# Optimization experiments

Measured on AMD Instinct MI355X. Metric: run time of the kernel, lower is better.

The kernel has to match this reference:

```python
import jax, jax.numpy as jnp
import numpy as np

B, T, N, CD, D = 8, 16, 256, 1280, 1024   # batch, frames, feats/frame, condition_dim, dim
H, DH, DEPTH, Q = 16, 64, 6, 16           # heads, dim_head, depth, latents per frame
FF = 4 * D


def setup_inputs() -> dict:
    key = jax.random.key(0)
    ks = iter(jax.random.split(key, 40))
    w = lambda shp: jax.random.normal(next(ks), shp, jnp.float32) * 0.02
    return dict(
        x_f=jax.random.normal(next(ks), (B, T, N, CD), jnp.float32),
        goal_w1=w((CD, 2 * D)), goal_b1=jnp.zeros((2 * D,), jnp.float32),
        goal_w2=w((2 * D, D)), goal_b2=jnp.zeros((D,), jnp.float32),
        latents=jax.random.normal(next(ks), (T, Q, D), jnp.float32),
        time_pos_emb=jax.random.normal(next(ks), (T, 1, D), jnp.float32),
        ln_media_g=jnp.ones((DEPTH, D), jnp.float32), ln_media_b=jnp.zeros((DEPTH, D), jnp.float32),
        ln_lat_g=jnp.ones((DEPTH, D), jnp.float32), ln_lat_b=jnp.zeros((DEPTH, D), jnp.float32),
        wq=w((DEPTH, D, H * DH)), wk=w((DEPTH, D, H * DH)), wv=w((DEPTH, D, H * DH)),
        wo=w((DEPTH, H * DH, D)),
        ffn_ln_g=jnp.ones((DEPTH, D), jnp.float32), ffn_ln_b=jnp.zeros((DEPTH, D), jnp.float32),
        ffn_w1=w((DEPTH, D, FF)), ffn_b1=jnp.zeros((DEPTH, FF), jnp.float32),
        ffn_w2=w((DEPTH, FF, D)), ffn_b2=jnp.zeros((DEPTH, D), jnp.float32),
        final_g=jnp.ones((D,), jnp.float32), final_b=jnp.zeros((D,), jnp.float32),
    )


def layer_norm(x, g, b, eps=1e-5):
    m = jnp.mean(x, axis=-1, keepdims=True)
    v = jnp.mean(jnp.square(x - m), axis=-1, keepdims=True)
    return (x - m) * jax.lax.rsqrt(v + eps) * g + b


def reference(x_f, goal_w1, goal_b1, goal_w2, goal_b2, latents, time_pos_emb,
              ln_media_g, ln_media_b, ln_lat_g, ln_lat_b, wq, wk, wv, wo,
              ffn_ln_g, ffn_ln_b, ffn_w1, ffn_b1, ffn_w2, ffn_b2, final_g, final_b):
    scale = DH ** -0.5
    # goal embedding: Linear -> GELU(exact) -> Linear, then add time positional embedding
    h = jax.nn.gelu(x_f @ goal_w1 + goal_b1, approximate=False) @ goal_w2 + goal_b2  # (B,T,N,D)
    h = h + time_pos_emb[None]                                                       # (T,1,D) broadcast
    feats = h.reshape(B * T, N, D)
    x = jnp.broadcast_to(latents[None], (B, T, Q, D)).reshape(B * T, Q, D)
    for i in range(DEPTH):
        f = layer_norm(feats, ln_media_g[i], ln_media_b[i])
        lat = layer_norm(x, ln_lat_g[i], ln_lat_b[i])
        q = (lat @ wq[i]).reshape(B * T, Q, H, DH).transpose(0, 2, 1, 3) * scale  # bhqd
        kv = jnp.concatenate([f, lat], axis=1)                                    # (BT, N+Q, D)
        k = (kv @ wk[i]).reshape(B * T, N + Q, H, DH).transpose(0, 2, 1, 3)       # bhfd
        v = (kv @ wv[i]).reshape(B * T, N + Q, H, DH).transpose(0, 2, 1, 3)
        sim = jnp.einsum('bhqd,bhfd->bhqf', q, k)
        alphas = jax.nn.softmax(sim, axis=-1)  # matches amax-subtract + softmax
        o = jnp.einsum('bhqf,bhfd->bhqd', alphas, v)
        o = o.transpose(0, 2, 1, 3).reshape(B * T, Q, H * DH)
        x = x + o @ wo[i]
        y = layer_norm(x, ffn_ln_g[i], ffn_ln_b[i])
        x = x + jax.nn.gelu(y @ ffn_w1[i] + ffn_b1[i], approximate=False) @ ffn_w2[i] + ffn_b2[i]
    x = x.reshape(B, T * Q, D)
    return layer_norm(x, final_g, final_b)
```

## Files before the change

kernel.cpp:

```cpp
#include <hip/hip_runtime.h>
#include <math.h>

#define DEV __device__ __forceinline__

typedef __attribute__((ext_vector_type(8))) short short8;
typedef __attribute__((ext_vector_type(4))) short short4v;
typedef __attribute__((ext_vector_type(4))) float f32x4;
typedef __attribute__((ext_vector_type(8))) __bf16 bf16x8;

DEV float bf2f(unsigned short u) {
    union { unsigned int i; float f; } c; c.i = ((unsigned int)u) << 16; return c.f;
}
DEV unsigned short f2bf(float f) {
    union { float f; unsigned int i; } c; c.f = f;
    unsigned int u = c.i;
    u += 0x7fffu + ((u >> 16) & 1u);
    return (unsigned short)(u >> 16);
}
DEV float gelu_exact(float x) { return 0.5f * x * (1.0f + erff(x * 0.70710678118654752f)); }

#define GLL16(g, l)                                                                   \
    __builtin_amdgcn_global_load_lds(                                                \
        (const __attribute__((address_space(1))) unsigned int*)(g),                  \
        (__attribute__((address_space(3))) unsigned int*)(l), 16, 0, 0)

__global__ __launch_bounds__(256)
void transpose_w(const float* __restrict__ in, unsigned short* __restrict__ out,
                 const float* __restrict__ rowscale, float uscale,
                 int K, int N, size_t inStride, size_t outStride, int scaleStride)
{
    __shared__ float tile[64][65];
    in  += (size_t)blockIdx.z * inStride;
    out += (size_t)blockIdx.z * outStride;
    const int k0 = blockIdx.y * 64, n0 = blockIdx.x * 64;
    const int tid = threadIdx.x;
    const int c = tid & 63;
#pragma unroll
    for (int i = 0; i < 16; ++i) {
        int rr = (i << 2) + (tid >> 6);
        float v = in[(size_t)(k0 + rr) * N + n0 + c];
        if (rowscale) v *= rowscale[(size_t)blockIdx.z * scaleStride + k0 + rr];
        tile[rr][c] = v * uscale;
    }
    __syncthreads();
#pragma unroll
    for (int i = 0; i < 16; ++i) {
        int rr = (i << 2) + (tid >> 6);
        out[(size_t)(n0 + rr) * K + k0 + c] = f2bf(tile[c][rr]);
    }
}

__global__ __launch_bounds__(256)
void fold_bias(const float* __restrict__ wk, const float* __restrict__ wv,
               const float* __restrict__ bmed, float* __restrict__ biaskv)
{
    const int d = blockIdx.x >> 3;
    const int rem = blockIdx.x & 7;
    const int part = rem >> 2;
    const int chunk = rem & 3;
    const float* w = (part ? wv : wk) + (size_t)d * 1024 * 1024 + chunk * 256 + threadIdx.x;
    const float* b = bmed + d * 1024;
    float acc = 0.f;
    for (int r = 0; r < 1024; ++r) acc += b[r] * w[(size_t)r * 1024];
    biaskv[d * 2048 + part * 1024 + chunk * 256 + threadIdx.x] = acc;
}

__global__ __launch_bounds__(256)
void convert_bf16(const float* __restrict__ in, unsigned short* __restrict__ out, size_t n4)
{
    size_t i = (size_t)blockIdx.x * 256 + threadIdx.x;
    if (i >= n4) return;
    float4 v = ((const float4*)in)[i];
    ushort4 u;
    u.x = f2bf(v.x); u.y = f2bf(v.y); u.z = f2bf(v.z); u.w = f2bf(v.w);
    ((ushort4*)out)[i] = u;
}

__global__ __launch_bounds__(256)
void init_x(const float* __restrict__ lat, float* __restrict__ x)
{
    const int row = blockIdx.x;
    ((float4*)x)[(size_t)row * 256 + threadIdx.x] =
        ((const float4*)lat)[(size_t)(row & 255) * 256 + threadIdx.x];
}

template<bool AFFINE, bool OUTBF>
__global__ __launch_bounds__(256)
void ln_k(const float* __restrict__ in, const float* __restrict__ g,
          const float* __restrict__ b, void* __restrict__ out)
{
    const int row = blockIdx.x;
    const int tid = threadIdx.x;
    float4 v = ((const float4*)(in + (size_t)row * 1024))[tid];
    float s  = v.x + v.y + v.z + v.w;
    float ss = v.x * v.x + v.y * v.y + v.z * v.z + v.w * v.w;
#pragma unroll
    for (int o = 32; o > 0; o >>= 1) { s += __shfl_down(s, o); ss += __shfl_down(ss, o); }
    __shared__ float red[8];
    if ((tid & 63) == 0) { red[tid >> 6] = s; red[4 + (tid >> 6)] = ss; }
    __syncthreads();
    const float sum  = red[0] + red[1] + red[2] + red[3];
    const float ssum = red[4] + red[5] + red[6] + red[7];
    const float mean = sum * (1.0f / 1024.0f);
    const float var  = ssum * (1.0f / 1024.0f) - mean * mean;
    const float rs   = rsqrtf(var + 1e-5f);
    float o0 = (v.x - mean) * rs, o1 = (v.y - mean) * rs;
    float o2 = (v.z - mean) * rs, o3 = (v.w - mean) * rs;
    if (AFFINE) {
        float4 gv = ((const float4*)g)[tid];
        float4 bv = ((const float4*)b)[tid];
        o0 = o0 * gv.x + bv.x; o1 = o1 * gv.y + bv.y;
        o2 = o2 * gv.z + bv.z; o3 = o3 * gv.w + bv.w;
    }
    if (OUTBF) {
        ushort4 u; u.x = f2bf(o0); u.y = f2bf(o1); u.z = f2bf(o2); u.w = f2bf(o3);
        ((ushort4*)out)[(size_t)row * 256 + tid] = u;
    } else {
        float4 ov; ov.x = o0; ov.y = o1; ov.z = o2; ov.w = o3;
        ((float4*)out)[(size_t)row * 256 + tid] = ov;
    }
}

enum { E_BF16 = 0, E_BIAS_BF16, E_BIAS_GELU_BF16, E_BIAS_TPOS_F32, E_ADD_F32, E_BIAS_ADD_F32 };

template<int EPI>
__global__ __launch_bounds__(256, 2)
void gemm_bt(const unsigned short* __restrict__ A, const unsigned short* __restrict__ Bt,
             void* __restrict__ Out,
             const float* __restrict__ bias, const float* __restrict__ addsrc,
             const float* __restrict__ tpos,
             int M, int N, int K)
{
    __shared__ unsigned short lds[2 * 128 * 64];
    const int tid  = threadIdx.x;
    const int wave = tid >> 6, lane = tid & 63;
    const int nbx  = N >> 7;

    const int nwg = gridDim.x;
    int bid = blockIdx.x;
    int wg = ((nwg & 7) == 0) ? ((bid & 7) * (nwg >> 3) + (bid >> 3)) : bid;
    const int by = wg / nbx, bx = wg % nbx;

    const int swz = ((lane & 7) ^ (lane >> 3)) * 8;
    const unsigned short* gA = A  + (size_t)(by * 128 + (lane >> 3)) * K + swz;
    const unsigned short* gB = Bt + (size_t)(bx * 128 + (lane >> 3)) * K + swz;

    const int wr = wave >> 1, wc = wave & 1;
    f32x4 acc[4][4] = {};

    unsigned short* ldsA = lds;
    unsigned short* ldsB = lds + 128 * 64;

    const int off0 = (((lane >> 4)    ) ^ (lane & 7)) * 8;
    const int off1 = (((lane >> 4) | 4) ^ (lane & 7)) * 8;
    const unsigned short* la = ldsA + (wr * 64 + (lane & 15)) * 64;
    const unsigned short* lb = ldsB + (wc * 64 + (lane & 15)) * 64;

    for (int kt = 0; kt < K; kt += 64) {
#pragma unroll
        for (int j = 0; j < 4; ++j) {
            const int chunk = (j << 2) + wave;
            GLL16(gA + (size_t)chunk * 8 * K + kt, ldsA + chunk * 512);
            GLL16(gB + (size_t)chunk * 8 * K + kt, ldsB + chunk * 512);
        }
        __syncthreads();
#pragma unroll
        for (int kk = 0; kk < 2; ++kk) {
            const int offk = kk ? off1 : off0;
            bf16x8 a[4], b[4];
#pragma unroll
            for (int m = 0; m < 4; ++m) a[m] = *(const bf16x8*)(la + m * 1024 + offk);
#pragma unroll
            for (int n = 0; n < 4; ++n) b[n] = *(const bf16x8*)(lb + n * 1024 + offk);
#pragma unroll
            for (int m = 0; m < 4; ++m)
#pragma unroll
                for (int n = 0; n < 4; ++n)
                    acc[m][n] = __builtin_amdgcn_mfma_f32_16x16x32_bf16(a[m], b[n], acc[m][n], 0, 0, 0);
        }
        __syncthreads();
    }

    const int r0 = by * 128 + wr * 64 + (lane >> 4) * 4;
    const int c0 = bx * 128 + wc * 64 + (lane & 15);
#pragma unroll
    for (int m = 0; m < 4; ++m) {
#pragma unroll
        for (int n = 0; n < 4; ++n) {
            const int c = c0 + n * 16;
#pragma unroll
            for (int j = 0; j < 4; ++j) {
                const int r = r0 + m * 16 + j;
                float v = acc[m][n][j];
                if (EPI == E_BIAS_BF16 || EPI == E_BIAS_GELU_BF16 ||
                    EPI == E_BIAS_TPOS_F32 || EPI == E_BIAS_ADD_F32)
                    v += bias[c];
                if (EPI == E_BIAS_GELU_BF16) v = gelu_exact(v);
                if (EPI == E_BIAS_TPOS_F32)  v += tpos[(((unsigned)r >> 8) & 15) * 1024 + c];
                if (EPI == E_ADD_F32 || EPI == E_BIAS_ADD_F32) v += addsrc[(size_t)r * N + c];
                if (EPI == E_BIAS_TPOS_F32 || EPI == E_ADD_F32 || EPI == E_BIAS_ADD_F32)
                    ((float*)Out)[(size_t)r * N + c] = v;
                else
                    ((unsigned short*)Out)[(size_t)r * N + c] = f2bf(v);
            }
        }
    }
}

template<int EPI>
__global__ __launch_bounds__(256, 4)
void gemm64(const unsigned short* __restrict__ A, const unsigned short* __restrict__ Bt,
            void* __restrict__ Out,
            const float* __restrict__ bias, const float* __restrict__ addsrc,
            int M, int N, int K)
{
    __shared__ unsigned short lds[64 * 64 + 128 * 64];
    const int tid  = threadIdx.x;
    const int wave = tid >> 6, lane = tid & 63;
    const int nbx  = N >> 7;

    const int nwg = gridDim.x;
    int bid = blockIdx.x;
    int wg = ((nwg & 7) == 0) ? ((bid & 7) * (nwg >> 3) + (bid >> 3)) : bid;
    const int by = wg / nbx, bx = wg % nbx;

    const int swz = ((lane & 7) ^ (lane >> 3)) * 8;
    const unsigned short* gA = A  + (size_t)(by * 64  + (lane >> 3)) * K + swz;
    const unsigned short* gB = Bt + (size_t)(bx * 128 + (lane >> 3)) * K + swz;

    const int wr = wave >> 1, wc = wave & 1;
    f32x4 acc[2][4] = {};

    unsigned short* ldsA = lds;
    unsigned short* ldsB = lds + 64 * 64;

    const int off0 = (((lane >> 4)    ) ^ (lane & 7)) * 8;
    const int off1 = (((lane >> 4) | 4) ^ (lane & 7)) * 8;
    const unsigned short* la = ldsA + (wr * 32 + (lane & 15)) * 64;
    const unsigned short* lb = ldsB + (wc * 64 + (lane & 15)) * 64;

    for (int kt = 0; kt < K; kt += 64) {
        GLL16(gA + (size_t)(wave)     * 8 * K + kt, ldsA + (wave)      * 512);
        GLL16(gA + (size_t)(4 + wave) * 8 * K + kt, ldsA + (4 + wave)  * 512);
#pragma unroll
        for (int j = 0; j < 4; ++j) {
            const int chunk = (j << 2) + wave;
            GLL16(gB + (size_t)chunk * 8 * K + kt, ldsB + chunk * 512);
        }
        __syncthreads();
#pragma unroll
        for (int kk = 0; kk < 2; ++kk) {
            const int offk = kk ? off1 : off0;
            bf16x8 a[2], b[4];
#pragma unroll
            for (int m = 0; m < 2; ++m) a[m] = *(const bf16x8*)(la + m * 1024 + offk);
#pragma unroll
            for (int n = 0; n < 4; ++n) b[n] = *(const bf16x8*)(lb + n * 1024 + offk);
#pragma unroll
            for (int m = 0; m < 2; ++m)
#pragma unroll
                for (int n = 0; n < 4; ++n)
                    acc[m][n] = __builtin_amdgcn_mfma_f32_16x16x32_bf16(a[m], b[n], acc[m][n], 0, 0, 0);
        }
        __syncthreads();
    }

    const int r0 = by * 64 + wr * 32 + (lane >> 4) * 4;
    const int c0 = bx * 128 + wc * 64 + (lane & 15);
#pragma unroll
    for (int m = 0; m < 2; ++m) {
#pragma unroll
        for (int n = 0; n < 4; ++n) {
            const int c = c0 + n * 16;
#pragma unroll
            for (int j = 0; j < 4; ++j) {
                const int r = r0 + m * 16 + j;
                float v = acc[m][n][j];
                if (EPI == E_BIAS_BF16 || EPI == E_BIAS_GELU_BF16 || EPI == E_BIAS_ADD_F32)
                    v += bias[c];
                if (EPI == E_BIAS_GELU_BF16) v = gelu_exact(v);
                if (EPI == E_ADD_F32 || EPI == E_BIAS_ADD_F32) v += addsrc[(size_t)r * N + c];
                if (EPI == E_ADD_F32 || EPI == E_BIAS_ADD_F32)
                    ((float*)Out)[(size_t)r * N + c] = v;
                else
                    ((unsigned short*)Out)[(size_t)r * N + c] = f2bf(v);
            }
        }
    }
}

__global__ __launch_bounds__(256)
void attn_k(const unsigned short* __restrict__ qkvl, const unsigned short* __restrict__ kvm,
            unsigned short* __restrict__ o)
{
    __shared__ unsigned short kv[272 * 72];
    __shared__ float sim[16 * 273];
    __shared__ float qs[16 * 68];
    __shared__ float red[64];

    const int bt = blockIdx.x >> 4, h = blockIdx.x & 15;
    const int tid = threadIdx.x;
    const int lane = tid & 63, wave = tid >> 6;
    const int r = tid & 15, grp = tid >> 4;

    {
        const int qi = tid >> 4, d0 = (tid & 15) * 4;
        const unsigned short* src = qkvl + (size_t)(bt * 16 + qi) * 3072 + h * 64 + d0;
        qs[qi * 68 + d0 + 0] = bf2f(src[0]);
        qs[qi * 68 + d0 + 1] = bf2f(src[1]);
        qs[qi * 68 + d0 + 2] = bf2f(src[2]);
        qs[qi * 68 + d0 + 3] = bf2f(src[3]);
    }
#pragma unroll
    for (int i = 0; i < 9; ++i) {
        int idx = i * 256 + tid;
        if (idx < 2176) {
            int f = idx >> 3, cp = idx & 7;
            const unsigned short* src = (f < 256)
                ? kvm  + (size_t)(bt * 256 + f) * 2048 + h * 64 + cp * 8
                : qkvl + (size_t)(bt * 16 + (f - 256)) * 3072 + 1024 + h * 64 + cp * 8;
            *(short8*)&kv[f * 72 + cp * 8] = *(const short8*)src;
        }
    }
    __syncthreads();

    float p[17];
#pragma unroll
    for (int i = 0; i < 17; ++i) p[i] = 0.f;
#pragma unroll
    for (int d = 0; d < 64; d += 8) {
        float q8[8];
#pragma unroll
        for (int j = 0; j < 8; ++j) q8[j] = qs[r * 68 + d + j];
#pragma unroll
        for (int i = 0; i < 17; ++i) {
            short8 k8 = *(const short8*)&kv[(grp + i * 16) * 72 + d];
#pragma unroll
            for (int j = 0; j < 8; ++j) p[i] += q8[j] * bf2f((unsigned short)k8[j]);
        }
    }
    float mx = -3.0e38f;
#pragma unroll
    for (int i = 0; i < 17; ++i) mx = fmaxf(mx, p[i]);
    mx = fmaxf(mx, __shfl_xor(mx, 16));
    mx = fmaxf(mx, __shfl_xor(mx, 32));
    if (lane < 16) red[wave * 16 + lane] = mx;
    __syncthreads();
    const float rowmax = fmaxf(fmaxf(red[r], red[16 + r]), fmaxf(red[32 + r], red[48 + r]));

    float sm = 0.f;
#pragma unroll
    for (int i = 0; i < 17; ++i) { p[i] = __expf(p[i] - rowmax); sm += p[i]; }
    sm += __shfl_xor(sm, 16);
    sm += __shfl_xor(sm, 32);
#pragma unroll
    for (int i = 0; i < 17; ++i) sim[r * 273 + grp + i * 16] = p[i];
    __syncthreads();
    if (lane < 16) red[wave * 16 + lane] = sm;
#pragma unroll
    for (int i = 0; i < 9; ++i) {
        int idx = i * 256 + tid;
        if (idx < 2176) {
            int f = idx >> 3, cp = idx & 7;
            const unsigned short* src = (f < 256)
                ? kvm  + (size_t)(bt * 256 + f) * 2048 + 1024 + h * 64 + cp * 8
                : qkvl + (size_t)(bt * 16 + (f - 256)) * 3072 + 2048 + h * 64 + cp * 8;
            *(short8*)&kv[f * 72 + cp * 8] = *(const short8*)src;
        }
    }
    __syncthreads();
    const float inv = 1.0f / (red[r] + red[16 + r] + red[32 + r] + red[48 + r]);

    float o0 = 0.f, o1 = 0.f, o2 = 0.f, o3 = 0.f;
    for (int f = 0; f < 272; ++f) {
        float pv = sim[r * 273 + f];
        short4v v4 = *(const short4v*)&kv[f * 72 + grp * 4];
        o0 += pv * bf2f((unsigned short)v4[0]);
        o1 += pv * bf2f((unsigned short)v4[1]);
        o2 += pv * bf2f((unsigned short)v4[2]);
        o3 += pv * bf2f((unsigned short)v4[3]);
    }
    unsigned short* dst = o + (size_t)(bt * 16 + r) * 1024 + h * 64 + grp * 4;
    dst[0] = f2bf(o0 * inv);
    dst[1] = f2bf(o1 * inv);
    dst[2] = f2bf(o2 * inv);
    dst[3] = f2bf(o3 * inv);
}

extern "C" void kernel_launch(void* const* d_in, const int* in_sizes, int n_in,
                              void* d_out, int out_size, void* d_ws, size_t ws_size,
                              hipStream_t stream)
{
    const float* x_f      = (const float*)d_in[0];
    const float* goal_w1  = (const float*)d_in[1];
    const float* goal_b1  = (const float*)d_in[2];
    const float* goal_w2  = (const float*)d_in[3];
    const float* goal_b2  = (const float*)d_in[4];
    const float* latents  = (const float*)d_in[5];
    const float* tpos     = (const float*)d_in[6];
    const float* lnm_g    = (const float*)d_in[7];
    const float* lnm_b    = (const float*)d_in[8];
    const float* lnl_g    = (const float*)d_in[9];
    const float* lnl_b    = (const float*)d_in[10];
    const float* wq       = (const float*)d_in[11];
    const float* wk       = (const float*)d_in[12];
    const float* wv       = (const float*)d_in[13];
    const float* wo       = (const float*)d_in[14];
    const float* ffn_g    = (const float*)d_in[15];
    const float* ffn_b    = (const float*)d_in[16];
    const float* ffw1     = (const float*)d_in[17];
    const float* ffb1     = (const float*)d_in[18];
    const float* ffw2     = (const float*)d_in[19];
    const float* ffb2     = (const float*)d_in[20];
    const float* fin_g    = (const float*)d_in[21];
    const float* fin_b    = (const float*)d_in[22];

    char* ws = (char*)d_ws;
    size_t off = 0;
    auto alloc = [&](size_t bytes) -> char* {
        char* p = ws + off;
        off += (bytes + 255) & ~(size_t)255;
        return p;
    };
    typedef unsigned short u16;
    u16*   wg1t   = (u16*)  alloc(2048ull * 1280 * 2);
    u16*   wg2t   = (u16*)  alloc(1024ull * 2048 * 2);
    u16*   wqkvl  = (u16*)  alloc(6ull * 3072 * 1024 * 2);
    u16*   wkvm   = (u16*)  alloc(6ull * 2048 * 1024 * 2);
    u16*   wot    = (u16*)  alloc(6ull * 1024 * 1024 * 2);
    u16*   wf1t   = (u16*)  alloc(6ull * 4096 * 1024 * 2);
    u16*   wf2t   = (u16*)  alloc(6ull * 1024 * 4096 * 2);
    float* biaskv = (float*)alloc(6ull * 2048 * 4);
    float* xres   = (float*)alloc(2048ull * 1024 * 4);
    u16*   latn   = (u16*)  alloc(2048ull * 1024 * 2);
    u16*   qkvl   = (u16*)  alloc(2048ull * 3072 * 2);
    u16*   obuf   = (u16*)  alloc(2048ull * 1024 * 2);
    u16*   ffny   = (u16*)  alloc(2048ull * 1024 * 2);
    u16*   ffnmid = (u16*)  alloc(2048ull * 4096 * 2);
    u16*   bufA   = (u16*)  alloc(32768ull * 2048 * 2);
    float* bufB   = (float*)alloc(32768ull * 1024 * 4);
    u16*   bufC   = (u16*)  alloc(41943040ull * 2);
    if (off > ws_size) return;

    convert_bf16<<<40960, 256, 0, stream>>>(x_f, bufC, 41943040ull / 4);
    transpose_w<<<dim3(32, 20, 1), 256, 0, stream>>>(goal_w1, wg1t, nullptr, 1.f, 1280, 2048, 0, 0, 0);
    transpose_w<<<dim3(16, 32, 1), 256, 0, stream>>>(goal_w2, wg2t, nullptr, 1.f, 2048, 1024, 0, 0, 0);
    transpose_w<<<dim3(16, 16, 6), 256, 0, stream>>>(wq, wqkvl,                nullptr, 0.125f, 1024, 1024, 1024ull*1024, 3072ull*1024, 0);
    transpose_w<<<dim3(16, 16, 6), 256, 0, stream>>>(wk, wqkvl + 1024ull*1024, nullptr, 1.f,    1024, 1024, 1024ull*1024, 3072ull*1024, 0);
    transpose_w<<<dim3(16, 16, 6), 256, 0, stream>>>(wv, wqkvl + 2048ull*1024, nullptr, 1.f,    1024, 1024, 1024ull*1024, 3072ull*1024, 0);
    transpose_w<<<dim3(16, 16, 6), 256, 0, stream>>>(wk, wkvm,                 lnm_g,   1.f,    1024, 1024, 1024ull*1024, 2048ull*1024, 1024);
    transpose_w<<<dim3(16, 16, 6), 256, 0, stream>>>(wv, wkvm + 1024ull*1024,  lnm_g,   1.f,    1024, 1024, 1024ull*1024, 2048ull*1024, 1024);
    transpose_w<<<dim3(16, 16, 6), 256, 0, stream>>>(wo, wot,                  nullptr, 1.f,    1024, 1024, 1024ull*1024, 1024ull*1024, 0);
    transpose_w<<<dim3(64, 16, 6), 256, 0, stream>>>(ffw1, wf1t,               nullptr, 1.f,    1024, 4096, 4096ull*1024, 4096ull*1024, 0);
    transpose_w<<<dim3(16, 64, 6), 256, 0, stream>>>(ffw2, wf2t,               nullptr, 1.f,    4096, 1024, 4096ull*1024, 4096ull*1024, 0);
    fold_bias<<<48, 256, 0, stream>>>(wk, wv, lnm_b, biaskv);
    init_x<<<2048, 256, 0, stream>>>(latents, xres);

    gemm_bt<E_BIAS_GELU_BF16><<<256 * 16, 256, 0, stream>>>(bufC, wg1t, bufA, goal_b1, nullptr, nullptr, 32768, 2048, 1280);
    gemm_bt<E_BIAS_TPOS_F32><<<256 * 8, 256, 0, stream>>>(bufA, wg2t, bufB, goal_b2, nullptr, tpos, 32768, 1024, 2048);
    ln_k<false, true><<<32768, 256, 0, stream>>>(bufB, nullptr, nullptr, bufC);

    for (int i = 0; i < 6; ++i) {
        const u16* wqkvl_i = wqkvl + (size_t)i * 3072 * 1024;
        const u16* wkvm_i  = wkvm  + (size_t)i * 2048 * 1024;
        const u16* wot_i   = wot   + (size_t)i * 1024 * 1024;
        const u16* wf1_i   = wf1t  + (size_t)i * 4096 * 1024;
        const u16* wf2_i   = wf2t  + (size_t)i * 1024 * 4096;

        ln_k<true, true><<<2048, 256, 0, stream>>>(xres, lnl_g + i * 1024, lnl_b + i * 1024, latn);
        gemm64<E_BF16><<<32 * 24, 256, 0, stream>>>(latn, wqkvl_i, qkvl, nullptr, nullptr, 2048, 3072, 1024);
        gemm_bt<E_BIAS_BF16><<<256 * 16, 256, 0, stream>>>(bufC, wkvm_i, bufA, biaskv + i * 2048, nullptr, nullptr, 32768, 2048, 1024);
        attn_k<<<2048, 256, 0, stream>>>(qkvl, bufA, obuf);
        gemm64<E_ADD_F32><<<32 * 8, 256, 0, stream>>>(obuf, wot_i, xres, nullptr, xres, 2048, 1024, 1024);
        ln_k<true, true><<<2048, 256, 0, stream>>>(xres, ffn_g + i * 1024, ffn_b + i * 1024, ffny);
        gemm64<E_BIAS_GELU_BF16><<<32 * 32, 256, 0, stream>>>(ffny, wf1_i, ffnmid, ffb1 + i * 4096, nullptr, 2048, 4096, 1024);
        gemm64<E_BIAS_ADD_F32><<<32 * 8, 256, 0, stream>>>(ffnmid, wf2_i, xres, ffb2 + i * 1024, xres, 2048, 1024, 4096);
    }

    ln_k<true, false><<<2048, 256, 0, stream>>>(xres, fin_g, fin_b, d_out);
}
```

Measured before the change: 2.825 ms.

## Replace 128x128 GEMM with 256x256 eight-wave ping-pong pipelined GEMM

Replaces the large-M bf16 GEMM kernel (goal embedding and per-layer media K/V projections) with a 256x256-tile, 512-thread kernel. It double-buffers LDS with async global-to-LDS loads issued two k-tiles ahead, splits each k-step into four phases with barriers and raised MFMA priority, and hoists the bias load out of the inner epilogue loop. The goal is to overlap memory traffic with MFMA work and raise arithmetic intensity. In exchange it uses 128KB of LDS and more accumulator registers per thread, which may limit occupancy. The hand-placed vmcnt waits also have to be exactly right for correctness.

```diff
diff --git a/kernel.cpp b/kernel.cpp
--- a/kernel.cpp
+++ b/kernel.cpp
@@ -19,10 +19,17 @@
 }
 DEV float gelu_exact(float x) { return 0.5f * x * (1.0f + erff(x * 0.70710678118654752f)); }
 
+DEV f32x4 MF(bf16x8 a, bf16x8 b, f32x4 c) {
+    return __builtin_amdgcn_mfma_f32_16x16x32_bf16(a, b, c, 0, 0, 0);
+}
+
 #define GLL16(g, l)                                                                   \
     __builtin_amdgcn_global_load_lds(                                                \
         (const __attribute__((address_space(1))) unsigned int*)(g),                  \
         (__attribute__((address_space(3))) unsigned int*)(l), 16, 0, 0)
+
+#define BAR()   __builtin_amdgcn_s_barrier()
+#define LGKM0() asm volatile("s_waitcnt lgkmcnt(0)" ::: "memory")
 
 __global__ __launch_bounds__(256)
 void transpose_w(const float* __restrict__ in, unsigned short* __restrict__ out,
@@ -124,84 +131,137 @@
 enum { E_BF16 = 0, E_BIAS_BF16, E_BIAS_GELU_BF16, E_BIAS_TPOS_F32, E_ADD_F32, E_BIAS_ADD_F32 };
 
 template<int EPI>
-__global__ __launch_bounds__(256, 2)
-void gemm_bt(const unsigned short* __restrict__ A, const unsigned short* __restrict__ Bt,
-             void* __restrict__ Out,
-             const float* __restrict__ bias, const float* __restrict__ addsrc,
-             const float* __restrict__ tpos,
-             int M, int N, int K)
-{
-    __shared__ unsigned short lds[2 * 128 * 64];
-    const int tid  = threadIdx.x;
-    const int wave = tid >> 6, lane = tid & 63;
-    const int nbx  = N >> 7;
-
+__global__ __launch_bounds__(512, 2)
+void g8p(const unsigned short* __restrict__ A, const unsigned short* __restrict__ Bt,
+         void* __restrict__ Out,
+         const float* __restrict__ bias, const float* __restrict__ tpos,
+         int M, int N, int K)
+{
+    __shared__ unsigned short sm[65536];
+
+    const int tid = threadIdx.x;
+    const int wid = tid >> 6, lane = tid & 63;
+    const int wm = wid >> 2, wn = wid & 3;
+
+    const int nbx = N >> 8;
     const int nwg = gridDim.x;
-    int bid = blockIdx.x;
-    int wg = ((nwg & 7) == 0) ? ((bid & 7) * (nwg >> 3) + (bid >> 3)) : bid;
+    const int bid = blockIdx.x;
+    const int wg = (bid & 7) * (nwg >> 3) + (bid >> 3);
     const int by = wg / nbx, bx = wg % nbx;
-
-    const int swz = ((lane & 7) ^ (lane >> 3)) * 8;
-    const unsigned short* gA = A  + (size_t)(by * 128 + (lane >> 3)) * K + swz;
-    const unsigned short* gB = Bt + (size_t)(bx * 128 + (lane >> 3)) * K + swz;
-
-    const int wr = wave >> 1, wc = wave & 1;
-    f32x4 acc[4][4] = {};
-
-    unsigned short* ldsA = lds;
-    unsigned short* ldsB = lds + 128 * 64;
-
-    const int off0 = (((lane >> 4)    ) ^ (lane & 7)) * 8;
-    const int off1 = (((lane >> 4) | 4) ^ (lane & 7)) * 8;
-    const unsigned short* la = ldsA + (wr * 64 + (lane & 15)) * 64;
-    const unsigned short* lb = ldsB + (wc * 64 + (lane & 15)) * 64;
-
-    for (int kt = 0; kt < K; kt += 64) {
-#pragma unroll
-        for (int j = 0; j < 4; ++j) {
-            const int chunk = (j << 2) + wave;
-            GLL16(gA + (size_t)chunk * 8 * K + kt, ldsA + chunk * 512);
-            GLL16(gB + (size_t)chunk * 8 * K + kt, ldsB + chunk * 512);
-        }
-        __syncthreads();
-#pragma unroll
-        for (int kk = 0; kk < 2; ++kk) {
-            const int offk = kk ? off1 : off0;
-            bf16x8 a[4], b[4];
-#pragma unroll
-            for (int m = 0; m < 4; ++m) a[m] = *(const bf16x8*)(la + m * 1024 + offk);
-#pragma unroll
-            for (int n = 0; n < 4; ++n) b[n] = *(const bf16x8*)(lb + n * 1024 + offk);
-#pragma unroll
-            for (int m = 0; m < 4; ++m)
-#pragma unroll
-                for (int n = 0; n < 4; ++n)
-                    acc[m][n] = __builtin_amdgcn_mfma_f32_16x16x32_bf16(a[m], b[n], acc[m][n], 0, 0, 0);
-        }
-        __syncthreads();
-    }
-
-    const int r0 = by * 128 + wr * 64 + (lane >> 4) * 4;
-    const int c0 = bx * 128 + wc * 64 + (lane & 15);
-#pragma unroll
-    for (int m = 0; m < 4; ++m) {
-#pragma unroll
-        for (int n = 0; n < 4; ++n) {
-            const int c = c0 + n * 16;
+    const int nt = K >> 6;
+
+    const int srow = wid * 8 + (lane >> 3);
+    const int schk = ((lane & 7) ^ (lane >> 3)) * 8;
+    const unsigned short* gA = A  + (size_t)(by * 256 + srow) * K + schk;
+    const unsigned short* gB = Bt + (size_t)(bx * 256 + srow) * K + schk;
+    const int ldst = wid * 512;
+
+    auto stgA = [&](int d, int h, int T) {
+        const unsigned short* g = gA + (size_t)(h * 64) * K + (size_t)T * 64;
+        unsigned short* l = sm + d * 16384 + h * 8192 + ldst;
+        GLL16(g, l);
+        GLL16(g + (size_t)128 * K, l + 4096);
+    };
+    auto stgB = [&](int d, int h, int T) {
+        const unsigned short* g = gB + (size_t)(h * 128) * K + (size_t)T * 64;
+        unsigned short* l = sm + 32768 + d * 16384 + h * 8192 + ldst;
+        GLL16(g, l);
+        GLL16(g + (size_t)64 * K, l + 4096);
+    };
+
+    const int q = lane >> 4;
+    const int cks0 = ((q    ) ^ (lane & 7)) * 8;
+    const int cks1 = ((q + 4) ^ (lane & 7)) * 8;
+    const int arow = (wm * 64 + (lane & 15)) * 64;
+    const int brow = ((wn & 1) * 64 + (lane & 15)) * 64;
+    const int bhoff = 32768 + (wn >> 1) * 8192;
+
+    f32x4 acc[8][4] = {};
+    bf16x8 a[2][2], b[4][2];
+
+    stgA(0, 0, 0); stgA(0, 1, 0); stgB(0, 0, 0); stgB(0, 1, 0);
+    if (nt > 1) { stgB(1, 0, 1); stgA(1, 0, 1); }
+    if (nt > 1) asm volatile("s_waitcnt vmcnt(4)" ::: "memory");
+    else        asm volatile("s_waitcnt vmcnt(0)" ::: "memory");
+    BAR();
+
+#define PH_READ_A(HOFF, E0)                                                      \
+    a[0][0] = *(const bf16x8*)(Ab + (HOFF) + arow + (E0) * 1024 + cks0);         \
+    a[0][1] = *(const bf16x8*)(Ab + (HOFF) + arow + (E0) * 1024 + cks1);         \
+    a[1][0] = *(const bf16x8*)(Ab + (HOFF) + arow + ((E0) + 1) * 1024 + cks0);   \
+    a[1][1] = *(const bf16x8*)(Ab + (HOFF) + arow + ((E0) + 1) * 1024 + cks1);
+
+#define PH_MFMA(R0)                                                              \
+    __builtin_amdgcn_s_setprio(1);                                               \
+    _Pragma("unroll")                                                            \
+    for (int e = 0; e < 2; ++e)                                                  \
+        _Pragma("unroll")                                                        \
+        for (int ni = 0; ni < 4; ++ni) {                                         \
+            acc[(R0) + e][ni] = MF(a[e][0], b[ni][0], acc[(R0) + e][ni]);        \
+            acc[(R0) + e][ni] = MF(a[e][1], b[ni][1], acc[(R0) + e][ni]);        \
+        }                                                                        \
+    __builtin_amdgcn_s_setprio(0);
+
+    for (int T = 0; T < nt; ++T) {
+        const int d = T & 1, dn = d ^ 1;
+        const unsigned short* Ab = sm + d * 16384;
+        const unsigned short* Bb = sm + bhoff + d * 16384;
+        const bool s1 = (T + 1 < nt), s2 = (T + 2 < nt);
+
+        PH_READ_A(0, 0);
+#pragma unroll
+        for (int ni = 0; ni < 4; ++ni) {
+            b[ni][0] = *(const bf16x8*)(Bb + brow + ni * 1024 + cks0);
+            b[ni][1] = *(const bf16x8*)(Bb + brow + ni * 1024 + cks1);
+        }
+        if (s1) { stgB(dn, 1, T + 1); stgA(dn, 1, T + 1); }
+        BAR(); LGKM0();
+        PH_MFMA(0);
+        BAR();
+
+        PH_READ_A(0, 2);
+        if (s2) stgB(d, 0, T + 2);
+        BAR(); LGKM0();
+        PH_MFMA(2);
+        BAR();
+
+        PH_READ_A(8192, 0);
+        if (s2) stgA(d, 0, T + 2);
+        BAR(); LGKM0();
+        PH_MFMA(4);
+        BAR();
+
+        PH_READ_A(8192, 2);
+        BAR(); LGKM0();
+        PH_MFMA(6);
+        if (s2)      asm volatile("s_waitcnt vmcnt(4)" ::: "memory");
+        else if (s1) asm volatile("s_waitcnt vmcnt(0)" ::: "memory");
+        BAR();
+    }
+#undef PH_READ_A
+#undef PH_MFMA
+
+    const int r0 = by * 256 + wm * 128 + (lane >> 4) * 4;
+    const int c0 = bx * 256 + wn * 64 + (lane & 15);
+#pragma unroll
+    for (int mi = 0; mi < 8; ++mi) {
+#pragma unroll
+        for (int ni = 0; ni < 4; ++ni) {
+            const int c = c0 + ni * 16;
+            float bv = 0.f;
+            if (EPI == E_BIAS_BF16 || EPI == E_BIAS_GELU_BF16 || EPI == E_BIAS_TPOS_F32)
+                bv = bias[c];
 #pragma unroll
             for (int j = 0; j < 4; ++j) {
-                const int r = r0 + m * 16 + j;
-                float v = acc[m][n][j];
-                if (EPI == E_BIAS_BF16 || EPI == E_BIAS_GELU_BF16 ||
-                    EPI == E_BIAS_TPOS_F32 || EPI == E_BIAS_ADD_F32)
-                    v += bias[c];
+                const int r = r0 + mi * 16 + j;
+                float v = acc[mi][ni][j] + bv;
                 if (EPI == E_BIAS_GELU_BF16) v = gelu_exact(v);
-                if (EPI == E_BIAS_TPOS_F32)  v += tpos[(((unsigned)r >> 8) & 15) * 1024 + c];
-                if (EPI == E_ADD_F32 || EPI == E_BIAS_ADD_F32) v += addsrc[(size_t)r * N + c];
-                if (EPI == E_BIAS_TPOS_F32 || EPI == E_ADD_F32 || EPI == E_BIAS_ADD_F32)
+                if (EPI == E_BIAS_TPOS_F32) {
+                    v += tpos[(((unsigned)r >> 8) & 15) * 1024 + c];
                     ((float*)Out)[(size_t)r * N + c] = v;
-                else
+                } else {
                     ((unsigned short*)Out)[(size_t)r * N + c] = f2bf(v);
+                }
             }
         }
     }
@@ -456,8 +516,8 @@
     fold_bias<<<48, 256, 0, stream>>>(wk, wv, lnm_b, biaskv);
     init_x<<<2048, 256, 0, stream>>>(latents, xres);
 
-    gemm_bt<E_BIAS_GELU_BF16><<<256 * 16, 256, 0, stream>>>(bufC, wg1t, bufA, goal_b1, nullptr, nullptr, 32768, 2048, 1280);
-    gemm_bt<E_BIAS_TPOS_F32><<<256 * 8, 256, 0, stream>>>(bufA, wg2t, bufB, goal_b2, nullptr, tpos, 32768, 1024, 2048);
+    g8p<E_BIAS_GELU_BF16><<<1024, 512, 0, stream>>>(bufC, wg1t, bufA, goal_b1, nullptr, 32768, 2048, 1280);
+    g8p<E_BIAS_TPOS_F32><<<512, 512, 0, stream>>>(bufA, wg2t, bufB, goal_b2, tpos, 32768, 1024, 2048);
     ln_k<false, true><<<32768, 256, 0, stream>>>(bufB, nullptr, nullptr, bufC);
 
     for (int i = 0; i < 6; ++i) {
@@ -469,7 +529,7 @@
 
         ln_k<true, true><<<2048, 256, 0, stream>>>(xres, lnl_g + i * 1024, lnl_b + i * 1024, latn);
         gemm64<E_BF16><<<32 * 24, 256, 0, stream>>>(latn, wqkvl_i, qkvl, nullptr, nullptr, 2048, 3072, 1024);
-        gemm_bt<E_BIAS_BF16><<<256 * 16, 256, 0, stream>>>(bufC, wkvm_i, bufA, biaskv + i * 2048, nullptr, nullptr, 32768, 2048, 1024);
+        g8p<E_BIAS_BF16><<<1024, 512, 0, stream>>>(bufC, wkvm_i, bufA, biaskv + i * 2048, nullptr, 32768, 2048, 1024);
         attn_k<<<2048, 256, 0, stream>>>(qkvl, bufA, obuf);
         gemm64<E_ADD_F32><<<32 * 8, 256, 0, stream>>>(obuf, wot_i, xres, nullptr, xres, 2048, 1024, 1024);
         ln_k<true, true><<<2048, 256, 0, stream>>>(xres, ffn_g + i * 1024, ffn_b + i * 1024, ffny);
```

After: 2.771 ms. About the same (-1.9%).
